# Kernel tuning notes

Hardware: AMD Instinct MI355X
Metric: run time of the kernel (lower is better)

The kernel has to match this reference:

```python
import jax, jax.numpy as jnp
import numpy as np

# Quantization / crossbar-simulation hyperparameters (from args)
WLA = 8          # wl_activate / wl_input bits
WLW = 8          # wl_weight bits
CELLBIT = 2      # bits stored per memory cell
ADC = 6          # ADC precision bits
SUB = 128        # crossbar subArray rows
ONOFF = 10.0     # cell on/off conductance ratio
STRIDE = 2
EPS = 1e-5


def _ste_round(v):
    return v + jax.lax.stop_gradient(jnp.round(v) - v)


def setup_inputs() -> dict:
    key = jax.random.key(0)
    ks = jax.random.split(key, 7)
    B, C, H, W, O = 16, 512, 28, 28, 1024
    x = jax.random.normal(ks[0], (B, C, H, W), dtype=jnp.float32)
    y = jax.random.normal(ks[1], (B, O, H // STRIDE, W // STRIDE), dtype=jnp.float32)
    bn_gamma = 1.0 + 0.1 * jax.random.normal(ks[2], (C,), dtype=jnp.float32)
    bn_beta = 0.1 * jax.random.normal(ks[3], (C,), dtype=jnp.float32)
    bn_mean = 0.1 * jax.random.normal(ks[4], (C,), dtype=jnp.float32)
    bn_var = jax.random.uniform(ks[5], (C,), dtype=jnp.float32, minval=0.5, maxval=1.5)
    w = 0.05 * jax.random.normal(ks[6], (O, C, 1, 1), dtype=jnp.float32)
    return {"x": x, "y": y, "bn_gamma": bn_gamma, "bn_beta": bn_beta,
            "bn_mean": bn_mean, "bn_var": bn_var, "w": w}


def _shortcut_q(x, y, bn_gamma, bn_beta, bn_mean, bn_var, w):
    # BatchNorm (inference, running stats) + ReLU
    inv = jax.lax.rsqrt(bn_var + EPS)
    xh = jax.nn.relu((x - bn_mean[None, :, None, None]) * (inv * bn_gamma)[None, :, None, None]
                     + bn_beta[None, :, None, None])

    aQ = float(2 ** WLA - 1)
    wQ = float(2 ** (WLW - 1) - 1)
    SHIFT = 2 ** (WLW - 1)  # map signed int weights to unsigned cells

    # Activation quantization to WLA unsigned bits (post-ReLU, per-tensor scale)
    a_max = jnp.maximum(jnp.max(xh), 1e-8)
    x_int = _ste_round(jnp.clip(xh / a_max, 0.0, 1.0) * aQ)          # [B,C,H,W] in [0, 255]
    xs = x_int[:, :, ::STRIDE, ::STRIDE]                              # 1x1 conv, stride 2

    # Weight quantization to WLW signed bits (per-tensor scale)
    w2 = w[:, :, 0, 0]                                                # [O,C]
    w_max = jnp.maximum(jnp.max(jnp.abs(w2)), 1e-8)
    w_int = _ste_round(jnp.clip(w2 / w_max, -1.0, 1.0) * wQ)          # [-127, 127]

    # Ideal integer conv (used for STE backward path)
    ideal = jnp.einsum('oc,bchw->bohw', w_int, xs)

    # --- analog crossbar simulation: bit-sliced inputs x cell-sliced weights + ADC ---
    cellRange = 2 ** CELLBIT
    nsl = WLW // CELLBIT
    off = (cellRange - 1) / (ONOFF - 1.0)                             # min-conductance offset
    B, C, Ho, Wo = xs.shape
    O = w2.shape[0]
    G = C // SUB                                                      # subarray groups along rows
    xg = xs.reshape(B, G, SUB, Ho, Wo)
    wu = (w_int + float(SHIFT)).reshape(O, G, SUB)                    # unsigned cell values
    vmax = SUB * (cellRange - 1 + off)                                # max per-column analog sum
    delta = vmax / float(2 ** ADC - 1)                                # ADC LSB

    sim = jnp.zeros_like(ideal)
    for z in range(WLA):                                              # input bit planes
        xb = jnp.floor(xg / (2.0 ** z)) % 2.0                         # [B,G,S,Ho,Wo] in {0,1}
        xsum = xb.sum(axis=2)                                         # dummy-column input [B,G,Ho,Wo]
        for k in range(nsl):                                          # weight cell slices
            wk = jnp.floor(wu / float(cellRange ** k)) % cellRange + off   # [O,G,S]
            dk = float((SHIFT // cellRange ** k) % cellRange) + off        # dummy cell value
            psum = jnp.einsum('ogs,bgshw->bgohw', wk, xb)             # analog column sums
            psum_q = jnp.round(psum / delta) * delta                  # ADC quantization
            dummy_q = jnp.round(dk * xsum / delta) * delta            # ADC on dummy column
            sim = sim + (2.0 ** z) * (float(cellRange) ** k) * (psum_q - dummy_q[:, :, None]).sum(axis=1)

    # STE: forward = simulated, backward = ideal quantized conv
    out_int = ideal + jax.lax.stop_gradient(sim - ideal)
    return out_int * (w_max / wQ) * (a_max / aQ) + y


def reference(x, y, bn_gamma, bn_beta, bn_mean, bn_var, w):
    return _shortcut_q(x, y, bn_gamma, bn_beta, bn_mean, bn_var, w)
```

## Files before the change

kernel.cpp:

```cpp
#include <hip/hip_runtime.h>
#include <math.h>

typedef __attribute__((ext_vector_type(4))) int i32x4;
typedef __attribute__((ext_vector_type(16))) int i32x16;

namespace {
constexpr int N_ = 3136;
constexpr int M_ = N_ * 8;
constexpr size_t FIN_OFF   = 0;
constexpr size_t AMAXP_OFF = 256;
constexpr size_t WMAXP_OFF = 4096;
constexpr size_t CHS_OFF   = 6144;
constexpr size_t DUM_OFF   = 8192;
constexpr size_t ACT_OFF   = 32768;
constexpr size_t WGT_OFF   = ACT_OFF + (size_t)M_ * 512;
}

__device__ __forceinline__ void gload(const char* g, char* l) {
  __builtin_amdgcn_global_load_lds(
      (const __attribute__((address_space(1))) char*)g,
      (__attribute__((address_space(3))) char*)l, 16, 0, 0);
}

__global__ __launch_bounds__(256) void prep1_kernel(
    const float* __restrict__ x, const float* __restrict__ w,
    const float* __restrict__ gamma, const float* __restrict__ beta,
    const float* __restrict__ mean, const float* __restrict__ var,
    float* __restrict__ amaxp, float* __restrict__ wmaxp, float* __restrict__ chs) {
#pragma clang fp contract(off)
  __shared__ float red[4];
  const int bx = blockIdx.x, tid = threadIdx.x;
  if (bx < 896) {
    int id = bx * 256 + tid;
    int row = id / 28;
    int seg = id - row * 28;
    int c = row & 511;
    const float4* p = (const float4*)(x + (size_t)row * 784 + seg * 28);
    float mn = 1e30f, mx = -1e30f;
#pragma unroll
    for (int i = 0; i < 7; ++i) {
      float4 v = p[i];
      mn = fminf(mn, fminf(fminf(v.x, v.y), fminf(v.z, v.w)));
      mx = fmaxf(mx, fmaxf(fmaxf(v.x, v.y), fmaxf(v.z, v.w)));
    }
    float vf = var[c] + 1e-5f;
    float sc = (float)(1.0 / sqrt((double)vf)) * gamma[c];
    float f1 = (mn - mean[c]) * sc + beta[c];
    float f2 = (mx - mean[c]) * sc + beta[c];
    float m = fmaxf(fmaxf(f1, f2), 0.f);
#pragma unroll
    for (int o = 32; o > 0; o >>= 1) m = fmaxf(m, __shfl_down(m, o, 64));
    if ((tid & 63) == 0) red[tid >> 6] = m;
    __syncthreads();
    if (tid == 0) amaxp[bx] = fmaxf(fmaxf(red[0], red[1]), fmaxf(red[2], red[3]));
  } else if (bx < 1152) {
    int id = (bx - 896) * 256 + tid;
    const float4* p = (const float4*)w + (size_t)id * 2;
    float4 v0 = p[0], v1 = p[1];
    float m = fmaxf(fmaxf(fmaxf(fabsf(v0.x), fabsf(v0.y)), fmaxf(fabsf(v0.z), fabsf(v0.w))),
                    fmaxf(fmaxf(fabsf(v1.x), fabsf(v1.y)), fmaxf(fabsf(v1.z), fabsf(v1.w))));
#pragma unroll
    for (int o = 32; o > 0; o >>= 1) m = fmaxf(m, __shfl_down(m, o, 64));
    if ((tid & 63) == 0) red[tid >> 6] = m;
    __syncthreads();
    if (tid == 0) wmaxp[bx - 896] = fmaxf(fmaxf(red[0], red[1]), fmaxf(red[2], red[3]));
  } else {
    int c = (bx - 1152) * 256 + tid;
    float vf = var[c] + 1e-5f;
    chs[c] = (float)(1.0 / sqrt((double)vf)) * gamma[c];
  }
}

__global__ __launch_bounds__(256) void pack_xw_kernel(
    const float* __restrict__ x, const float* __restrict__ mean,
    const float* __restrict__ beta, const float* __restrict__ chs,
    const float* __restrict__ amaxp, const float* __restrict__ w,
    const float* __restrict__ wmaxp, unsigned* __restrict__ act,
    unsigned* __restrict__ wgt, float* __restrict__ fin) {
#pragma clang fp contract(off)
  const int bx = blockIdx.x, tid = threadIdx.x;
  if (bx < 448) {
    __shared__ float samax;
    __shared__ unsigned char sx[14 * 256];
    const int chalf = bx & 1;
    const int bh = bx >> 1;
    const int b = bh / 14, h2 = bh - b * 14;
    if (tid < 64) {
      float m = 0.f;
      for (int i = tid; i < 896; i += 64) m = fmaxf(m, amaxp[i]);
#pragma unroll
      for (int o = 32; o > 0; o >>= 1) m = fmaxf(m, __shfl_down(m, o, 64));
      if (tid == 0) {
        float a = fmaxf(m, 1e-8f);
        samax = a;
        if (bx == 0) fin[0] = a;
      }
    }
    __syncthreads();
    const float amax = samax;
    const int cbase = chalf * 256;
    for (int it = 0; it < 7; ++it) {
      int id = it * 256 + tid;
      int cl = id / 7, q = id - cl * 7;
      int c = cbase + cl;
      const float4 v = *(const float4*)(x + (size_t)(b * 512 + c) * 784 + h2 * 56 + q * 4);
      float sc = chs[c], mu = mean[c], be = beta[c];
      float f0 = fmaxf((v.x - mu) * sc + be, 0.f);
      int i0 = (int)rintf(fminf(fmaxf(f0 / amax, 0.f), 1.f) * 255.0f);
      float f2 = fmaxf((v.z - mu) * sc + be, 0.f);
      int i2 = (int)rintf(fminf(fmaxf(f2 / amax, 0.f), 1.f) * 255.0f);
      sx[(2 * q) * 256 + cl] = (unsigned char)i0;
      sx[(2 * q + 1) * 256 + cl] = (unsigned char)i2;
    }
    __syncthreads();
    const int nbase = b * 196 + h2 * 14;
    for (int it = 0; it < 4; ++it) {
      int id = it * 256 + tid;
      if (id < 896) {
        int cql = id & 63, w2 = id >> 6;
        unsigned v = *(const unsigned*)(sx + w2 * 256 + cql * 4);
        int n = nbase + w2;
        int cq = chalf * 64 + cql;
        int g = cq >> 5, j = (cq & 31) >> 3, kh = (cq >> 2) & 1, bp = cq & 3;
        size_t base = (size_t)(n >> 2) * 16384 +
                      (size_t)(g * 4 + j) * 1024 + kh * 512 + bp * 4;
        int rowin0 = (n * 8) & 31;
#pragma unroll
        for (int z = 0; z < 8; ++z)
          act[(base + (rowin0 + z) * 16) >> 2] = (v >> z) & 0x01010101u;
      }
    }
  } else {
    __shared__ float swmax;
    const int bx2 = bx - 448;
    if (tid < 64) {
      float m = fmaxf(fmaxf(wmaxp[tid], wmaxp[tid + 64]),
                      fmaxf(wmaxp[tid + 128], wmaxp[tid + 192]));
#pragma unroll
      for (int o = 32; o > 0; o >>= 1) m = fmaxf(m, __shfl_down(m, o, 64));
      if (tid == 0) {
        float a = fmaxf(m, 1e-8f);
        swmax = a;
        if (bx2 == 0) fin[1] = a;
      }
    }
    __syncthreads();
    const float wmax = swmax;
    int t = bx2 * 256 + tid;
    int c16 = t & 31, k = (t >> 5) & 3, o = t >> 7;
    unsigned words[4];
#pragma unroll
    for (int q = 0; q < 4; ++q) {
      unsigned wd = 0;
#pragma unroll
      for (int j = 0; j < 4; ++j) {
        int c = c16 * 16 + q * 4 + j;
        float v = fminf(fmaxf(w[(size_t)o * 512 + c] / wmax, -1.f), 1.f);
        int wi = (int)rintf(v * 127.0f);
        unsigned wu = (unsigned)(wi + 128);
        unsigned cell = (wu >> (2 * k)) & 3u;
        wd |= (3u * cell + 1u) << (8 * j);
      }
      words[q] = wd;
    }
    int r = o * 4 + k;
    size_t off = (size_t)(r >> 6) * 32768 + (size_t)(c16 >> 2) * 4096 +
                 (size_t)(((c16 & 3) << 6) + (r & 63)) * 16;
    *(uint4*)(wgt + (off >> 2)) = make_uint4(words[0], words[1], words[2], words[3]);
  }
}

__global__ __launch_bounds__(256) void dummy_kernel(const char* __restrict__ act2,
                                                    int* __restrict__ dummy) {
  int id = blockIdx.x * 256 + threadIdx.x;
  int t = id >> 6, lane = id & 63;
  const char* p = act2 + (size_t)t * 16384 + lane * 16;
  int z = (t * 32 + (lane & 31)) & 7;
  int dterm = 0;
#pragma unroll
  for (int g = 0; g < 4; ++g) {
    int sg = 0;
#pragma unroll
    for (int j = 0; j < 4; ++j) {
      const uint4 v = *(const uint4*)(p + (g * 4 + j) * 1024);
      sg += __popc(v.x) + __popc(v.y) + __popc(v.z) + __popc(v.w);
    }
    int xs = sg + __shfl_xor(sg, 32, 64);
    unsigned q0 = (__umul24((unsigned)xs, 51610u) + 524288u) >> 20;
    unsigned q3 = (__umul24((unsigned)xs, 361268u) + 524288u) >> 20;
    dterm += (int)((__umul24(q0, 21u) + (q3 << 6)) << z);
  }
  dterm += __shfl_xor(dterm, 1, 64);
  dterm += __shfl_xor(dterm, 2, 64);
  dterm += __shfl_xor(dterm, 4, 64);
  if ((lane & 39) == 0)
    dummy[t * 4 + ((lane >> 3) & 3)] = dterm;
}


#define APREF(off_, p_) {                                   \
  av[p_][0] = *(const i32x4*)(gA + (off_));                 \
  av[p_][1] = *(const i32x4*)(gA + (off_) + 1024);          \
  av[p_][2] = *(const i32x4*)(gA + (off_) + 2048);          \
  av[p_][3] = *(const i32x4*)(gA + (off_) + 3072);          \
}

#define GCOMP(g_, p_) {                                                       \
  i32x4 b00 = *(const i32x4*)(rB + (g_) * 8192);                              \
  i32x4 b10 = *(const i32x4*)(rB + (g_) * 8192 + 512);                        \
  i32x16 c0 = __builtin_amdgcn_mfma_i32_32x32x32_i8(av[p_][0], b00, zvec, 0, 0, 0); \
  i32x16 c1 = __builtin_amdgcn_mfma_i32_32x32x32_i8(av[p_][0], b10, zvec, 0, 0, 0); \
  _Pragma("unroll")                                                           \
  for (int j = 1; j < 4; ++j) {                                               \
    i32x4 b0 = *(const i32x4*)(rB + (g_) * 8192 + j * 2048);                  \
    i32x4 b1 = *(const i32x4*)(rB + (g_) * 8192 + j * 2048 + 512);            \
    c0 = __builtin_amdgcn_mfma_i32_32x32x32_i8(av[p_][j], b0, c0, 0, 0, 0);   \
    c1 = __builtin_amdgcn_mfma_i32_32x32x32_i8(av[p_][j], b1, c1, 0, 0, 0);   \
  }                                                                           \
  _Pragma("unroll")                                                           \
  for (int e = 0; e < 16; ++e) {                                              \
    unsigned q0q = (__umul24((unsigned)c0[e], 51610u) + 524288u) >> 20;       \
    acc[0][e >> 2] += (int)(q0q << shr[e & 3]);                               \
    unsigned q1q = (__umul24((unsigned)c1[e], 51610u) + 524288u) >> 20;       \
    acc[1][e >> 2] += (int)(q1q << shr[e & 3]);                               \
  }                                                                           \
}

#define GUNIT(i_, g_, pref_) {                                                \
  const int p_ = ((i_) * 4 + (g_)) & 1;                                       \
  if (pref_) {                                                                \
    const int nu = (i_) * 4 + (g_) + 1;                                       \
    APREF((nu >> 2) * 65536 + (nu & 3) * 4096, 1 - p_)                        \
  }                                                                           \
  GCOMP(g_, p_)                                                               \
}

#define MBLK_EPI(i_) {                                                        \
  int sums[2][4];                                                             \
  _Pragma("unroll")                                                           \
  for (int cs = 0; cs < 2; ++cs)                                              \
    _Pragma("unroll")                                                         \
    for (int cc = 0; cc < 4; ++cc) {                                          \
      int v = acc[cs][cc];                                                    \
      v += __shfl_xor(v, 1, 64);                                              \
      v += __shfl_xor(v, 2, 64);                                              \
      v += __shfl_xor(v, 32, 64);                                             \
      sums[cs][cc] = v;                                                       \
      acc[cs][cc] = 0;                                                        \
    }                                                                         \
  if ((lane & 3) == 0 && lane < 32) {                                         \
    const int ol = lane >> 2;                                                 \
    _Pragma("unroll")                                                         \
    for (int cc = 0; cc < 4; ++cc) {                                          \
      int n = (mslice * 4 + (i_)) * 16 + wm * 4 + cc;                         \
      int d = dp[n];                                                          \
      int b = n / 196, hw = n - b * 196;                                      \
      _Pragma("unroll")                                                       \
      for (int cs = 0; cs < 2; ++cs) {                                        \
        int o = cblk * 16 + cs * 8 + ol;                                      \
        size_t idx = ((size_t)(b * 1024 + o)) * 196 + hw;                     \
        out[idx] = (float)(sums[cs][cc] - d) * scale + y[idx];                \
      }                                                                       \
    }                                                                         \
  }                                                                           \
}

#define MBLK(i_, last_) {                                                     \
  GUNIT(i_, 0, 1) GUNIT(i_, 1, 1) GUNIT(i_, 2, 1) GUNIT(i_, 3, !(last_))     \
  MBLK_EPI(i_)                                                                \
}

__global__ __launch_bounds__(256, 4) void shortcutq_main_kernel(
    const char* __restrict__ act, const char* __restrict__ wgt,
    const int* __restrict__ dp, const float* __restrict__ y,
    const float* __restrict__ fin, float* __restrict__ out) {
  __shared__ __align__(16) char lds[32768];
  const int tid = threadIdx.x;
  const int cblk = blockIdx.x;
  const int mslice = blockIdx.y;
  const int lane = tid & 63, wm = tid >> 6;

  const char* gA = act + (size_t)(mslice * 16 + wm) * 16384 + lane * 16;
  const char* gB = wgt + (size_t)cblk * 32768 + tid * 16;
  const char* rB = lds + (lane >> 5) * 1024 + (lane & 31) * 16;

  const int shb = 4 * (lane >> 5) + 2 * (lane & 3);
  int shr[4] = {shb, shb + 1, shb + 2, shb + 3};

  i32x4 av[2][4];
  int acc[2][4];
#pragma unroll
  for (int cs = 0; cs < 2; ++cs)
#pragma unroll
    for (int cc = 0; cc < 4; ++cc) acc[cs][cc] = 0;
  i32x16 zvec;
#pragma unroll
  for (int e = 0; e < 16; ++e) zvec[e] = 0;

  APREF(0, 0)
#pragma unroll
  for (int l = 0; l < 8; ++l)
    gload(gB + l * 4096, lds + l * 4096 + tid * 16);
  __syncthreads();

  const float scale = (float)((128.0 * (3.0 + 1.0 / 3.0)) / 63.0) *
                      (fin[1] / 127.0f) * (fin[0] / 255.0f);

  MBLK(0, 0) MBLK(1, 0) MBLK(2, 0) MBLK(3, 1)
}

extern "C" void kernel_launch(void* const* d_in, const int* in_sizes, int n_in,
                              void* d_out, int out_size, void* d_ws, size_t ws_size,
                              hipStream_t stream) {
  const float* x     = (const float*)d_in[0];
  const float* y     = (const float*)d_in[1];
  const float* gamma = (const float*)d_in[2];
  const float* beta  = (const float*)d_in[3];
  const float* mean  = (const float*)d_in[4];
  const float* var   = (const float*)d_in[5];
  const float* w     = (const float*)d_in[6];
  float* out = (float*)d_out;

  char* wsb = (char*)d_ws;
  float* fin    = (float*)(wsb + FIN_OFF);
  float* amaxp  = (float*)(wsb + AMAXP_OFF);
  float* wmaxp  = (float*)(wsb + WMAXP_OFF);
  float* chs    = (float*)(wsb + CHS_OFF);
  int*   dum    = (int*)(wsb + DUM_OFF);
  char*  actb   = wsb + ACT_OFF;
  char*  wgtb   = wsb + WGT_OFF;

  hipLaunchKernelGGL(prep1_kernel, dim3(1154), dim3(256), 0, stream,
                     x, w, gamma, beta, mean, var, amaxp, wmaxp, chs);
  hipLaunchKernelGGL(pack_xw_kernel, dim3(960), dim3(256), 0, stream,
                     x, mean, beta, chs, amaxp, w, wmaxp,
                     (unsigned*)actb, (unsigned*)wgtb, fin);
  hipLaunchKernelGGL(dummy_kernel, dim3(196), dim3(256), 0, stream, actb, dum);
  hipLaunchKernelGGL(shortcutq_main_kernel, dim3(64, 49), dim3(256), 0, stream,
                     actb, wgtb, dum, y, fin, out);
}
```

Before: 180.2 us.

## Fuse dummy-column computation into activation packing and vectorize bit-plane stores

Removes the separate dummy kernel and computes per-pixel dummy-column ADC terms inside the activation pack kernel from the LDS-staged bytes. Each pack block now covers 28 pixels (4 tiles) and writes full 16-byte bit-plane rows instead of scattered 4-byte stores. Partial dummy sums per channel half go to a doubled buffer that the main kernel adds in its epilogue. This saves one launch and a full re-read of the packed activation buffer, but uses more LDS and fewer, larger blocks.

Result: no change. 179.3 us (-0.5%).

```diff
diff --git a/kernel.cpp b/kernel.cpp
--- a/kernel.cpp
+++ b/kernel.cpp
@@ -12,7 +12,7 @@
 constexpr size_t WMAXP_OFF = 4096;
 constexpr size_t CHS_OFF   = 6144;
 constexpr size_t DUM_OFF   = 8192;
-constexpr size_t ACT_OFF   = 32768;
+constexpr size_t ACT_OFF   = 36864;
 constexpr size_t WGT_OFF   = ACT_OFF + (size_t)M_ * 512;
 }
 
@@ -76,15 +76,17 @@
     const float* __restrict__ beta, const float* __restrict__ chs,
     const float* __restrict__ amaxp, const float* __restrict__ w,
     const float* __restrict__ wmaxp, unsigned* __restrict__ act,
-    unsigned* __restrict__ wgt, float* __restrict__ fin) {
+    unsigned* __restrict__ wgt, int* __restrict__ dummy_part,
+    float* __restrict__ fin) {
 #pragma clang fp contract(off)
   const int bx = blockIdx.x, tid = threadIdx.x;
-  if (bx < 448) {
+  if (bx < 224) {
     __shared__ float samax;
-    __shared__ unsigned char sx[14 * 256];
+    __shared__ __align__(16) unsigned char sx[28 * 256];
+    __shared__ int dd[448];
     const int chalf = bx & 1;
-    const int bh = bx >> 1;
-    const int b = bh / 14, h2 = bh - b * 14;
+    const int bp = (bx >> 1) % 7;
+    const int b = (bx >> 1) / 7;
     if (tid < 64) {
       float m = 0.f;
       for (int i = tid; i < 896; i += 64) m = fmaxf(m, amaxp[i]);
@@ -98,41 +100,66 @@
     }
     __syncthreads();
     const float amax = samax;
-    const int cbase = chalf * 256;
-    for (int it = 0; it < 7; ++it) {
+    for (int it = 0; it < 14; ++it) {
       int id = it * 256 + tid;
-      int cl = id / 7, q = id - cl * 7;
-      int c = cbase + cl;
-      const float4 v = *(const float4*)(x + (size_t)(b * 512 + c) * 784 + h2 * 56 + q * 4);
+      int cl = id / 14, r = id - cl * 14;
+      int rowsel = r / 7, f4i = r - rowsel * 7;
+      int c = chalf * 256 + cl;
+      const float4 v = *(const float4*)(
+          x + (size_t)(b * 512 + c) * 784 + (bp * 4 + 2 * rowsel) * 28 + f4i * 4);
       float sc = chs[c], mu = mean[c], be = beta[c];
       float f0 = fmaxf((v.x - mu) * sc + be, 0.f);
       int i0 = (int)rintf(fminf(fmaxf(f0 / amax, 0.f), 1.f) * 255.0f);
       float f2 = fmaxf((v.z - mu) * sc + be, 0.f);
       int i2 = (int)rintf(fminf(fmaxf(f2 / amax, 0.f), 1.f) * 255.0f);
-      sx[(2 * q) * 256 + cl] = (unsigned char)i0;
-      sx[(2 * q + 1) * 256 + cl] = (unsigned char)i2;
-    }
-    __syncthreads();
-    const int nbase = b * 196 + h2 * 14;
-    for (int it = 0; it < 4; ++it) {
+      int nl = rowsel * 14 + f4i * 2;
+      sx[nl * 256 + cl] = (unsigned char)i0;
+      sx[(nl + 1) * 256 + cl] = (unsigned char)i2;
+    }
+    __syncthreads();
+    const int tile0 = (b * 196 + 28 * bp) >> 2;
+    for (int it = 0; it < 14; ++it) {
       int id = it * 256 + tid;
-      if (id < 896) {
-        int cql = id & 63, w2 = id >> 6;
-        unsigned v = *(const unsigned*)(sx + w2 * 256 + cql * 4);
-        int n = nbase + w2;
-        int cq = chalf * 64 + cql;
-        int g = cq >> 5, j = (cq & 31) >> 3, kh = (cq >> 2) & 1, bp = cq & 3;
-        size_t base = (size_t)(n >> 2) * 16384 +
-                      (size_t)(g * 4 + j) * 1024 + kh * 512 + bp * 4;
-        int rowin0 = (n * 8) & 31;
-#pragma unroll
-        for (int z = 0; z < 8; ++z)
-          act[(base + (rowin0 + z) * 16) >> 2] = (v >> z) & 0x01010101u;
+      int row = id & 31, kh = (id >> 5) & 1, gjl = (id >> 6) & 7, tilel = id >> 9;
+      int nl = tilel * 4 + (row >> 3), z = row & 7;
+      int cl0 = (gjl >> 2) * 128 + (gjl & 3) * 32 + kh * 16;
+      const uint4 v = *(const uint4*)(sx + nl * 256 + cl0);
+      uint4 o;
+      o.x = (v.x >> z) & 0x01010101u;
+      o.y = (v.y >> z) & 0x01010101u;
+      o.z = (v.z >> z) & 0x01010101u;
+      o.w = (v.w >> z) & 0x01010101u;
+      size_t off = (size_t)(tile0 + tilel) * 16384 +
+                   (size_t)(chalf * 8 + gjl) * 1024 + kh * 512 + row * 16;
+      *(uint4*)((char*)act + off) = o;
+    }
+    for (int it = 0; it < 2; ++it) {
+      int id = it * 256 + tid;
+      if (id < 448) {
+        int z = id & 7, gl = (id >> 3) & 1, nl = id >> 4;
+        const unsigned* sw = (const unsigned*)(sx + nl * 256 + gl * 128);
+        int xs = 0;
+#pragma unroll
+        for (int wq = 0; wq < 8; ++wq) {
+          uint4 vv = *(const uint4*)(sw + wq * 4);
+          xs += __popc((vv.x >> z) & 0x01010101u) + __popc((vv.y >> z) & 0x01010101u) +
+                __popc((vv.z >> z) & 0x01010101u) + __popc((vv.w >> z) & 0x01010101u);
+        }
+        unsigned q0 = (__umul24((unsigned)xs, 51610u) + 524288u) >> 20;
+        unsigned q3 = (__umul24((unsigned)xs, 361268u) + 524288u) >> 20;
+        dd[id] = (int)((__umul24(q0, 21u) + (q3 << 6)) << z);
       }
+    }
+    __syncthreads();
+    if (tid < 28) {
+      int s = 0;
+#pragma unroll
+      for (int i = 0; i < 16; ++i) s += dd[tid * 16 + i];
+      dummy_part[(b * 196 + 28 * bp + tid) * 2 + chalf] = s;
     }
   } else {
     __shared__ float swmax;
-    const int bx2 = bx - 448;
+    const int bx2 = bx - 224;
     if (tid < 64) {
       float m = fmaxf(fmaxf(wmaxp[tid], wmaxp[tid + 64]),
                       fmaxf(wmaxp[tid + 128], wmaxp[tid + 192]));
@@ -168,33 +195,6 @@
                  (size_t)(((c16 & 3) << 6) + (r & 63)) * 16;
     *(uint4*)(wgt + (off >> 2)) = make_uint4(words[0], words[1], words[2], words[3]);
   }
-}
-
-__global__ __launch_bounds__(256) void dummy_kernel(const char* __restrict__ act2,
-                                                    int* __restrict__ dummy) {
-  int id = blockIdx.x * 256 + threadIdx.x;
-  int t = id >> 6, lane = id & 63;
-  const char* p = act2 + (size_t)t * 16384 + lane * 16;
-  int z = (t * 32 + (lane & 31)) & 7;
-  int dterm = 0;
-#pragma unroll
-  for (int g = 0; g < 4; ++g) {
-    int sg = 0;
-#pragma unroll
-    for (int j = 0; j < 4; ++j) {
-      const uint4 v = *(const uint4*)(p + (g * 4 + j) * 1024);
-      sg += __popc(v.x) + __popc(v.y) + __popc(v.z) + __popc(v.w);
-    }
-    int xs = sg + __shfl_xor(sg, 32, 64);
-    unsigned q0 = (__umul24((unsigned)xs, 51610u) + 524288u) >> 20;
-    unsigned q3 = (__umul24((unsigned)xs, 361268u) + 524288u) >> 20;
-    dterm += (int)((__umul24(q0, 21u) + (q3 << 6)) << z);
-  }
-  dterm += __shfl_xor(dterm, 1, 64);
-  dterm += __shfl_xor(dterm, 2, 64);
-  dterm += __shfl_xor(dterm, 4, 64);
-  if ((lane & 39) == 0)
-    dummy[t * 4 + ((lane >> 3) & 3)] = dterm;
 }
 
 
@@ -253,7 +253,7 @@
     _Pragma("unroll")                                                         \
     for (int cc = 0; cc < 4; ++cc) {                                          \
       int n = (mslice * 4 + (i_)) * 16 + wm * 4 + cc;                         \
-      int d = dp[n];                                                          \
+      int d = dp[n * 2] + dp[n * 2 + 1];                                      \
       int b = n / 196, hw = n - b * 196;                                      \
       _Pragma("unroll")                                                       \
       for (int cs = 0; cs < 2; ++cs) {                                        \
@@ -332,10 +332,9 @@
 
   hipLaunchKernelGGL(prep1_kernel, dim3(1154), dim3(256), 0, stream,
                      x, w, gamma, beta, mean, var, amaxp, wmaxp, chs);
-  hipLaunchKernelGGL(pack_xw_kernel, dim3(960), dim3(256), 0, stream,
+  hipLaunchKernelGGL(pack_xw_kernel, dim3(736), dim3(256), 0, stream,
                      x, mean, beta, chs, amaxp, w, wmaxp,
-                     (unsigned*)actb, (unsigned*)wgtb, fin);
-  hipLaunchKernelGGL(dummy_kernel, dim3(196), dim3(256), 0, stream, actb, dum);
+                     (unsigned*)actb, (unsigned*)wgtb, dum, fin);
   hipLaunchKernelGGL(shortcutq_main_kernel, dim3(64, 49), dim3(256), 0, stream,
                      actb, wgtb, dum, y, fin, out);
 }
```
